# Kernel tuning notes

Measured on AMD Instinct MI355X. Metric: run time of the kernel, lower is better.

Reference implementation:

```python
import jax, jax.numpy as jnp
import numpy as np

B, N, H, F = 256, 256, 256, 64   # batch, nodes, hidden, output
NNB = 4                          # neighbors per node (nns - 1)
HEADS = 3
S = 2 ** NNB - 1                 # nonempty subsets for Mobius Choquet
# MASK[s, i] = True iff neighbor i is in subset s (subsets 1..2^n-1)
MASK = jnp.asarray(np.array([[(s >> i) & 1 for i in range(NNB)] for s in range(1, S + 1)], dtype=bool))


def setup_inputs() -> dict:
    key = jax.random.key(0)
    ks = jax.random.split(key, 12)
    w = 0.02
    centers = jnp.arange(N, dtype=jnp.int64)[:, None]
    neigh = jax.random.randint(ks[11], (N, NNB), 0, N).astype(jnp.int64)
    local_edges = jnp.concatenate([centers, neigh], axis=1)[:, None, :]  # [N, 1, 5]
    return {
        "observation": jax.random.normal(ks[0], (B, N, H), jnp.float32),
        "action": jax.random.normal(ks[1], (B, N, H), jnp.float32),
        "V_W1": jax.random.normal(ks[2], (N, H, H), jnp.float32) * w,
        "V_b1": jnp.zeros((N, H), jnp.float32),
        "V_W2": jax.random.normal(ks[3], (N, H, F), jnp.float32) * w,
        "V_b2": jnp.zeros((N, F), jnp.float32),
        "A_W1": jax.random.normal(ks[4], (N, 2 * H, H), jnp.float32) * w,
        "A_b1": jnp.zeros((N, H), jnp.float32),
        "A_W2": jax.random.normal(ks[5], (N, H, F), jnp.float32) * w,
        "A_b2": jnp.zeros((N, F), jnp.float32),
        "chi_m": jax.random.normal(ks[6], (N, HEADS, S), jnp.float32) * w,
        "local_edges": local_edges,
    }


def _mmlp2(x, W1, b1, W2, b2):
    # per-node (multi) 2-layer MLP: first layer ReLU, second linear (act=False)
    h = jax.nn.relu(jnp.einsum('bni,nio->bno', x, W1) + b1)
    return jnp.einsum('bnh,nho->bno', h, W2) + b2


def reference(observation, action, V_W1, V_b1, V_W2, V_b2,
              A_W1, A_b1, A_W2, A_b2, chi_m, local_edges):
    V = _mmlp2(observation, V_W1, V_b1, V_W2, V_b2)                      # [B,N,F]
    A = _mmlp2(jnp.concatenate([observation, action], axis=-1),
               A_W1, A_b1, A_W2, A_b2)                                   # [B,N,F]
    Q = A + V                                                            # [B,N,F]
    centers = local_edges[:, 0, 0]        # [N]
    neigh = local_edges[:, 0, 1:]         # [N, NNB]
    # .data in torch -> detach the gathered neighbor Q-values
    Qn = jax.lax.stop_gradient(Q[:, neigh, :])                           # [B,N,NNB,F]
    # Mobius Choquet: min over each nonempty subset of neighbors
    masked = jnp.where(MASK[None, None, :, :, None], Qn[:, :, None, :, :], jnp.inf)
    mins = masked.min(axis=3)                                            # [B,N,S,F]
    chi = jnp.einsum('bnsf,nhs->bnf', mins, chi_m) / HEADS               # [B,N,F]
    return (chi + Q[:, centers, :]).mean(axis=-1)                        # [B,N]
```

## Files before the change

### kernel.cpp

```cpp
#include <hip/hip_runtime.h>
#include <cstddef>


#define BN 256
#define HD 256
#define FD 64
#define XS 40
#define SLS 268

typedef _Float16 f16x8 __attribute__((ext_vector_type(8)));
typedef _Float16 f16x4 __attribute__((ext_vector_type(4)));
typedef float f32x4 __attribute__((ext_vector_type(4)));

#define GLOAD16(g, l)                                              \
  __builtin_amdgcn_global_load_lds(                                \
      (__attribute__((address_space(1))) void*)(g),                \
      (__attribute__((address_space(3))) void*)(l), 16, 0, 0)

#define WAIT_BAR(VMCNT_STR)                                        \
  asm volatile("s_waitcnt " VMCNT_STR " lgkmcnt(0)" ::: "memory"); \
  __builtin_amdgcn_s_barrier();                                    \
  asm volatile("" ::: "memory");

__device__ __forceinline__ void x_load(const float* xs0, const float* xs1, int n,
                                       int kt, int tid, float4 xr[4]) {
  int kOff = kt * 32;
  const float* xs = (kOff < 256) ? xs0 : xs1;
  int l = tid & 63, w = tid >> 6;
  const float* base = xs + (size_t)n * HD + (kOff & 255) + (l & 7) * 4;
#pragma unroll
  for (int i = 0; i < 4; ++i) {
    int row = w * 32 + i * 8 + (l >> 3);
    xr[i] = *(const float4*)(base + (size_t)row * (BN * HD));
  }
}
__device__ __forceinline__ void x_write(_Float16* Xl, int tid, const float4 xr[4]) {
  int l = tid & 63, w = tid >> 6;
#pragma unroll
  for (int i = 0; i < 4; ++i) {
    int row = w * 32 + i * 8 + (l >> 3);
    f16x4 v;
    v[0] = (_Float16)xr[i].x; v[1] = (_Float16)xr[i].y;
    v[2] = (_Float16)xr[i].z; v[3] = (_Float16)xr[i].w;
    *(f16x4*)(Xl + row * XS + (l & 7) * 4) = v;
  }
}

__device__ __forceinline__ void w_gload(const float* Wg, float* Wl, int ktile,
                                        int w, int lane) {
#pragma unroll
  for (int s = 0; s < 4; ++s) {
    const float* src = Wg + (size_t)(ktile * 32 + w * 4 + s) * HD + lane * 4;
    float* dst = Wl + (w * 4 + s) * 256;
    GLOAD16(src, dst);
  }
}

__device__ __forceinline__ void g1_compute(const float* Wc, const _Float16* Xc,
                                           int lrow, int lk8, int Nbase, int wm1,
                                           f32x4 acc[8][4]) {
  f16x8 b[4];
#pragma unroll
  for (int nf = 0; nf < 4; ++nf) {
    const float* p = Wc + lk8 * 256 + Nbase + nf * 16 + lrow;
    f16x8 t;
#pragma unroll
    for (int j = 0; j < 8; ++j) t[j] = (_Float16)p[j * 256];
    b[nf] = t;
  }
#pragma unroll
  for (int m = 0; m < 8; ++m) {
    f16x8 a = *(const f16x8*)(Xc + (wm1 * 128 + m * 16 + lrow) * XS + lk8);
#pragma unroll
    for (int nf = 0; nf < 4; ++nf)
      acc[m][nf] = __builtin_amdgcn_mfma_f32_16x16x32_f16(a, b[nf], acc[m][nf], 0, 0, 0);
  }
}

template <int NK>
__device__ __forceinline__ void run_gemm1(const float* xs0, const float* xs1,
                                          const float* Wg, int n, int tid,
                                          int lrow, int lk8, int Nbase, int wm1,
                                          int w, int lane,
                                          float* Wl0, float* Wl1,
                                          _Float16* Xl0, _Float16* Xl1,
                                          f32x4 acc[8][4]) {
  float4 xrA[4], xrB[4];
  w_gload(Wg, Wl0, 0, w, lane);
  x_load(xs0, xs1, n, 0, tid, xrA);
  x_load(xs0, xs1, n, 1, tid, xrB);
  x_write(Xl0, tid, xrA);
  __syncthreads();
#pragma unroll 1
  for (int kt = 0; kt < NK - 2; kt += 2) {
    w_gload(Wg, Wl1, kt + 1, w, lane);
    x_load(xs0, xs1, n, kt + 2, tid, xrA);
    g1_compute(Wl0, Xl0, lrow, lk8, Nbase, wm1, acc);
    x_write(Xl1, tid, xrB);
    WAIT_BAR("vmcnt(4)")
    w_gload(Wg, Wl0, kt + 2, w, lane);
    x_load(xs0, xs1, n, kt + 3, tid, xrB);
    g1_compute(Wl1, Xl1, lrow, lk8, Nbase, wm1, acc);
    x_write(Xl0, tid, xrA);
    WAIT_BAR("vmcnt(4)")
  }
  w_gload(Wg, Wl1, NK - 1, w, lane);
  g1_compute(Wl0, Xl0, lrow, lk8, Nbase, wm1, acc);
  x_write(Xl1, tid, xrB);
  WAIT_BAR("vmcnt(0)")
  g1_compute(Wl1, Xl1, lrow, lk8, Nbase, wm1, acc);
}

__device__ __forceinline__ void gemm2_branch(f32x4 acc[8][4], f32x4 acc2[2][4],
                                             const float* W2g, const float* b1g,
                                             float* W_lds, _Float16* slab,
                                             int lrow, int lq, int lk8,
                                             int Nbase, int wm1, int wn1,
                                             int w, int lane) {
#pragma unroll
  for (int s = 0; s < 8; ++s) {
    int off = w * 2048 + s * 256;
    GLOAD16(W2g + off + lane * 4, W_lds + off);
  }
  float bv[4];
#pragma unroll
  for (int nf = 0; nf < 4; ++nf) bv[nf] = b1g[Nbase + nf * 16 + lrow];
#pragma unroll 1
  for (int s = 0; s < 4; ++s) {
    if (wn1 == s) {
#pragma unroll
      for (int m = 0; m < 8; ++m)
#pragma unroll
        for (int nf = 0; nf < 4; ++nf) {
          f16x4 hv;
#pragma unroll
          for (int r = 0; r < 4; ++r)
            hv[r] = (_Float16)fmaxf(acc[m][nf][r] + bv[nf], 0.f);
          *(f16x4*)(slab + (nf * 16 + lrow) * SLS + wm1 * 128 + m * 16 + lq * 4) = hv;
        }
    }
    __syncthreads();
#pragma unroll
    for (int kf = 0; kf < 2; ++kf) {
      f16x8 a[2], bb[4];
#pragma unroll
      for (int mf = 0; mf < 2; ++mf) {
        f16x8 t;
#pragma unroll
        for (int j = 0; j < 8; ++j)
          t[j] = slab[(kf * 32 + lk8 + j) * SLS + w * 32 + mf * 16 + lrow];
        a[mf] = t;
      }
#pragma unroll
      for (int nf = 0; nf < 4; ++nf) {
        const float* p = W_lds + (s * 64 + kf * 32 + lk8) * 64 + nf * 16 + lrow;
        f16x8 t;
#pragma unroll
        for (int j = 0; j < 8; ++j) t[j] = (_Float16)p[j * 64];
        bb[nf] = t;
      }
#pragma unroll
      for (int mf = 0; mf < 2; ++mf)
#pragma unroll
        for (int nf = 0; nf < 4; ++nf)
          acc2[mf][nf] =
              __builtin_amdgcn_mfma_f32_16x16x32_f16(a[mf], bb[nf], acc2[mf][nf], 0, 0, 0);
    }
    __syncthreads();
  }
}

__global__ __launch_bounds__(512, 2) void phase1_kernel(
    const float* __restrict__ obs, const float* __restrict__ act,
    const float* __restrict__ V_W1, const float* __restrict__ V_b1,
    const float* __restrict__ V_W2, const float* __restrict__ V_b2,
    const float* __restrict__ A_W1, const float* __restrict__ A_b1,
    const float* __restrict__ A_W2, const float* __restrict__ A_b2,
    float* __restrict__ Q) {
  __shared__ float W_lds[16384];
  __shared__ __align__(16) _Float16 Xl[2][256 * XS];
  __shared__ __align__(16) _Float16 slab[64 * SLS];
  float* Wl0 = W_lds;
  float* Wl1 = W_lds + 8192;

  int tid = threadIdx.x;
  int l = tid & 63, w = tid >> 6, lane = l;
  int lrow = l & 15, lq = l >> 4, lk8 = lq * 8;
  int wm1 = w >> 2, wn1 = w & 3;
  int Nbase = wn1 * 64;
  int n = blockIdx.x;

  f32x4 acc[8][4];
  f32x4 acc2[2][4];
#pragma unroll
  for (int i = 0; i < 2; ++i)
#pragma unroll
    for (int j = 0; j < 4; ++j) acc2[i][j] = (f32x4){0.f, 0.f, 0.f, 0.f};

#pragma unroll
  for (int m = 0; m < 8; ++m)
#pragma unroll
    for (int nf = 0; nf < 4; ++nf) acc[m][nf] = (f32x4){0.f, 0.f, 0.f, 0.f};
  run_gemm1<8>(obs, obs, V_W1 + (size_t)n * HD * HD, n, tid, lrow, lk8, Nbase,
               wm1, w, lane, Wl0, Wl1, Xl[0], Xl[1], acc);
  __syncthreads();
  gemm2_branch(acc, acc2, V_W2 + (size_t)n * HD * FD, V_b1 + n * HD,
               W_lds, slab, lrow, lq, lk8, Nbase, wm1, wn1, w, lane);

#pragma unroll
  for (int m = 0; m < 8; ++m)
#pragma unroll
    for (int nf = 0; nf < 4; ++nf) acc[m][nf] = (f32x4){0.f, 0.f, 0.f, 0.f};
  run_gemm1<16>(obs, act, A_W1 + (size_t)n * 2 * HD * HD, n, tid, lrow, lk8, Nbase,
                wm1, w, lane, Wl0, Wl1, Xl[0], Xl[1], acc);
  __syncthreads();
  gemm2_branch(acc, acc2, A_W2 + (size_t)n * HD * FD, A_b1 + n * HD,
               W_lds, slab, lrow, lq, lk8, Nbase, wm1, wn1, w, lane);

  const float* vb2 = V_b2 + n * FD;
  const float* ab2 = A_b2 + n * FD;
#pragma unroll
  for (int mf = 0; mf < 2; ++mf)
#pragma unroll
    for (int nf = 0; nf < 4; ++nf) {
      int f = nf * 16 + lrow;
      float bias = vb2[f] + ab2[f];
#pragma unroll
      for (int rr = 0; rr < 4; ++rr) {
        int row = w * 32 + mf * 16 + lq * 4 + rr;
        Q[(size_t)row * (BN * FD) + n * FD + f] = acc2[mf][nf][rr] + bias;
      }
    }
}

__global__ __launch_bounds__(256) void phase2_kernel(const float* __restrict__ Q,
                                                     const float* __restrict__ chi_m,
                                                     const int* __restrict__ le,
                                                     float* __restrict__ out) {
  int b = blockIdx.x;
  int n = threadIdx.x;
  int step = (le[5] == 1) ? 1 : 2;
  const int* e = le + n * 5 * step;
  int c  = e[0 * step] & (BN - 1);
  int n0 = e[1 * step] & (BN - 1);
  int n1 = e[2 * step] & (BN - 1);
  int n2 = e[3 * step] & (BN - 1);
  int n3 = e[4 * step] & (BN - 1);
  const float* ch = chi_m + n * 45;
  float cm[15];
#pragma unroll
  for (int s = 0; s < 15; ++s) cm[s] = (ch[s] + ch[15 + s] + ch[30 + s]) * (1.f / 3.f);
  const float* qb = Q + (size_t)b * (BN * FD);
  const float* q0 = qb + n0 * FD;
  const float* q1 = qb + n1 * FD;
  const float* q2 = qb + n2 * FD;
  const float* q3 = qb + n3 * FD;
  const float* qc = qb + c * FD;
  float acc = 0.f;
#pragma unroll
  for (int f = 0; f < FD; f += 4) {
    float4 v0 = *(const float4*)(q0 + f);
    float4 v1 = *(const float4*)(q1 + f);
    float4 v2 = *(const float4*)(q2 + f);
    float4 v3 = *(const float4*)(q3 + f);
    float4 vc = *(const float4*)(qc + f);
    const float* p0 = (const float*)&v0;
    const float* p1 = (const float*)&v1;
    const float* p2 = (const float*)&v2;
    const float* p3 = (const float*)&v3;
    const float* pc = (const float*)&vc;
#pragma unroll
    for (int u = 0; u < 4; ++u) {
      float a = p0[u], bq = p1[u], cq = p2[u], d = p3[u];
      float m01 = fminf(a, bq), m02 = fminf(a, cq), m03 = fminf(a, d);
      float m12 = fminf(bq, cq), m13 = fminf(bq, d), m23 = fminf(cq, d);
      float m012 = fminf(m01, cq), m013 = fminf(m01, d);
      float m023 = fminf(m02, d),  m123 = fminf(m12, d);
      float m0123 = fminf(m01, m23);
      float chi = cm[0] * a   + cm[1] * bq   + cm[2] * m01  + cm[3] * cq
                + cm[4] * m02 + cm[5] * m12  + cm[6] * m012 + cm[7] * d
                + cm[8] * m03 + cm[9] * m13  + cm[10] * m013 + cm[11] * m23
                + cm[12] * m023 + cm[13] * m123 + cm[14] * m0123;
      acc += chi + pc[u];
    }
  }
  out[b * BN + n] = acc * (1.f / 64.f);
}

extern "C" void kernel_launch(void* const* d_in, const int* in_sizes, int n_in,
                              void* d_out, int out_size, void* d_ws, size_t ws_size,
                              hipStream_t stream) {
  (void)in_sizes; (void)n_in; (void)out_size; (void)ws_size;
  const float* obs  = (const float*)d_in[0];
  const float* act  = (const float*)d_in[1];
  const float* V_W1 = (const float*)d_in[2];
  const float* V_b1 = (const float*)d_in[3];
  const float* V_W2 = (const float*)d_in[4];
  const float* V_b2 = (const float*)d_in[5];
  const float* A_W1 = (const float*)d_in[6];
  const float* A_b1 = (const float*)d_in[7];
  const float* A_W2 = (const float*)d_in[8];
  const float* A_b2 = (const float*)d_in[9];
  const float* chim = (const float*)d_in[10];
  const int*   le   = (const int*)d_in[11];
  float* Q   = (float*)d_ws;
  float* out = (float*)d_out;

  phase1_kernel<<<dim3(256), dim3(512), 0, stream>>>(obs, act, V_W1, V_b1, V_W2, V_b2,
                                                     A_W1, A_b1, A_W2, A_b2, Q);
  phase2_kernel<<<dim3(256), dim3(256), 0, stream>>>(Q, chim, le, out);
}
```

Baseline: 117.5 us.

## Use triple-buffered weight ring, prefetch W2 during GEMM1 tail, swizzle LDS

Measured after the change: 116.5 us. Within noise of the previous version (-0.9%).

```diff
diff --git a/kernel.cpp b/kernel.cpp
--- a/kernel.cpp
+++ b/kernel.cpp
@@ -46,26 +46,41 @@
   }
 }
 
-__device__ __forceinline__ void w_gload(const float* Wg, float* Wl, int ktile,
-                                        int w, int lane) {
+__device__ __forceinline__ void w1_gload(const float* __restrict__ Wg, float* Wl,
+                                         int ktile, int w, int lane) {
 #pragma unroll
   for (int s = 0; s < 4; ++s) {
-    const float* src = Wg + (size_t)(ktile * 32 + w * 4 + s) * HD + lane * 4;
-    float* dst = Wl + (w * 4 + s) * 256;
-    GLOAD16(src, dst);
+    int rl = w * 4 + s;
+    int swz = ((rl >> 3) & 3) << 4;
+    const float* src = Wg + (size_t)(ktile * 32 + rl) * HD + ((lane * 4) ^ swz);
+    GLOAD16(src, Wl + rl * HD);
+  }
+}
+
+__device__ __forceinline__ void w2_gload_half(const float* __restrict__ W2g, float* chunk,
+                                              int half, int w, int lane) {
+#pragma unroll
+  for (int s = 0; s < 4; ++s) {
+    int rl = (w * 4 + s) * 4;
+    int swz = ((rl >> 3) & 3) << 4;
+    const float* src = W2g + (size_t)(half * 128 + rl + (lane >> 4)) * FD
+                       + (((lane & 15) * 4) ^ swz);
+    GLOAD16(src, chunk + rl * FD);
   }
 }
 
 __device__ __forceinline__ void g1_compute(const float* Wc, const _Float16* Xc,
-                                           int lrow, int lk8, int Nbase, int wm1,
+                                           int lrow, int lq, int Nbase, int wm1,
                                            f32x4 acc[8][4]) {
+  int lk8 = lq * 8;
+  const float* wbase = Wc + lk8 * 256;
   f16x8 b[4];
 #pragma unroll
   for (int nf = 0; nf < 4; ++nf) {
-    const float* p = Wc + lk8 * 256 + Nbase + nf * 16 + lrow;
+    int col = (Nbase + nf * 16 + lrow) ^ (lq << 4);
     f16x8 t;
 #pragma unroll
-    for (int j = 0; j < 8; ++j) t[j] = (_Float16)p[j * 256];
+    for (int j = 0; j < 8; ++j) t[j] = (_Float16)wbase[j * 256 + col];
     b[nf] = t;
   }
 #pragma unroll
@@ -79,49 +94,56 @@
 
 template <int NK>
 __device__ __forceinline__ void run_gemm1(const float* xs0, const float* xs1,
-                                          const float* Wg, int n, int tid,
-                                          int lrow, int lk8, int Nbase, int wm1,
-                                          int w, int lane,
-                                          float* Wl0, float* Wl1,
-                                          _Float16* Xl0, _Float16* Xl1,
+                                          const float* __restrict__ Wg,
+                                          const float* __restrict__ W2g,
+                                          int n, int tid, int lrow, int lq,
+                                          int Nbase, int wm1, int w, int lane,
+                                          float* Wring, _Float16* Xl0, _Float16* Xl1,
                                           f32x4 acc[8][4]) {
+  float* w0 = Wring;
+  float* w1 = Wring + 8192;
+  float* w2 = Wring + 16384;
   float4 xrA[4], xrB[4];
-  w_gload(Wg, Wl0, 0, w, lane);
   x_load(xs0, xs1, n, 0, tid, xrA);
+  w1_gload(Wg, w0, 0, w, lane);
   x_load(xs0, xs1, n, 1, tid, xrB);
+  w1_gload(Wg, w1, 1, w, lane);
   x_write(Xl0, tid, xrA);
-  __syncthreads();
+  WAIT_BAR("vmcnt(8)")
 #pragma unroll 1
-  for (int kt = 0; kt < NK - 2; kt += 2) {
-    w_gload(Wg, Wl1, kt + 1, w, lane);
-    x_load(xs0, xs1, n, kt + 2, tid, xrA);
-    g1_compute(Wl0, Xl0, lrow, lk8, Nbase, wm1, acc);
-    x_write(Xl1, tid, xrB);
-    WAIT_BAR("vmcnt(4)")
-    w_gload(Wg, Wl0, kt + 2, w, lane);
-    x_load(xs0, xs1, n, kt + 3, tid, xrB);
-    g1_compute(Wl1, Xl1, lrow, lk8, Nbase, wm1, acc);
-    x_write(Xl0, tid, xrA);
-    WAIT_BAR("vmcnt(4)")
-  }
-  w_gload(Wg, Wl1, NK - 1, w, lane);
-  g1_compute(Wl0, Xl0, lrow, lk8, Nbase, wm1, acc);
-  x_write(Xl1, tid, xrB);
-  WAIT_BAR("vmcnt(0)")
-  g1_compute(Wl1, Xl1, lrow, lk8, Nbase, wm1, acc);
+  for (int kt = 0; kt < NK; kt += 2) {
+    if (kt + 2 < NK) {
+      x_load(xs0, xs1, n, kt + 2, tid, xrA);
+      w1_gload(Wg, w2, kt + 2, w, lane);
+    } else {
+      w2_gload_half(W2g, w2, 0, w, lane);
+    }
+    g1_compute(w0, Xl0, lrow, lq, Nbase, wm1, acc);
+    if (kt + 1 < NK) x_write(Xl1, tid, xrB);
+    if (kt < NK - 2) { WAIT_BAR("vmcnt(8)") }
+    else             { WAIT_BAR("vmcnt(4)") }
+    { float* t = w0; w0 = w1; w1 = w2; w2 = t; }
+    if (kt + 3 < NK) {
+      x_load(xs0, xs1, n, kt + 3, tid, xrB);
+      w1_gload(Wg, w2, kt + 3, w, lane);
+    } else {
+      w2_gload_half(W2g, w2, 1, w, lane);
+    }
+    g1_compute(w0, Xl1, lrow, lq, Nbase, wm1, acc);
+    if (kt + 2 < NK) {
+      x_write(Xl0, tid, xrA);
+      WAIT_BAR("vmcnt(8)")
+    }
+    { float* t = w0; w0 = w1; w1 = w2; w2 = t; }
+  }
 }
 
 __device__ __forceinline__ void gemm2_branch(f32x4 acc[8][4], f32x4 acc2[2][4],
-                                             const float* W2g, const float* b1g,
-                                             float* W_lds, _Float16* slab,
-                                             int lrow, int lq, int lk8,
-                                             int Nbase, int wm1, int wn1,
-                                             int w, int lane) {
-#pragma unroll
-  for (int s = 0; s < 8; ++s) {
-    int off = w * 2048 + s * 256;
-    GLOAD16(W2g + off + lane * 4, W_lds + off);
-  }
+                                             const float* cA, const float* cB,
+                                             const float* __restrict__ b1g,
+                                             _Float16* slab, int lrow, int lq,
+                                             int Nbase, int wm1, int wn1, int w) {
+  int lk8 = lq * 8;
   float bv[4];
 #pragma unroll
   for (int nf = 0; nf < 4; ++nf) bv[nf] = b1g[Nbase + nf * 16 + lrow];
@@ -142,21 +164,23 @@
     __syncthreads();
 #pragma unroll
     for (int kf = 0; kf < 2; ++kf) {
-      f16x8 a[2], bb[4];
+      const int r0 = s * 64 + kf * 32;
+      const float* wb2 = ((r0 < 128) ? cA : cB) + ((r0 & 127) + lk8) * FD;
+      f16x8 a2[2], bb[4];
 #pragma unroll
       for (int mf = 0; mf < 2; ++mf) {
         f16x8 t;
 #pragma unroll
         for (int j = 0; j < 8; ++j)
           t[j] = slab[(kf * 32 + lk8 + j) * SLS + w * 32 + mf * 16 + lrow];
-        a[mf] = t;
+        a2[mf] = t;
       }
 #pragma unroll
       for (int nf = 0; nf < 4; ++nf) {
-        const float* p = W_lds + (s * 64 + kf * 32 + lk8) * 64 + nf * 16 + lrow;
+        int col = (nf * 16 + lrow) ^ (lq << 4);
         f16x8 t;
 #pragma unroll
-        for (int j = 0; j < 8; ++j) t[j] = (_Float16)p[j * 64];
+        for (int j = 0; j < 8; ++j) t[j] = (_Float16)wb2[j * FD + col];
         bb[nf] = t;
       }
 #pragma unroll
@@ -164,7 +188,7 @@
 #pragma unroll
         for (int nf = 0; nf < 4; ++nf)
           acc2[mf][nf] =
-              __builtin_amdgcn_mfma_f32_16x16x32_f16(a[mf], bb[nf], acc2[mf][nf], 0, 0, 0);
+              __builtin_amdgcn_mfma_f32_16x16x32_f16(a2[mf], bb[nf], acc2[mf][nf], 0, 0, 0);
     }
     __syncthreads();
   }
@@ -177,15 +201,15 @@
     const float* __restrict__ A_W1, const float* __restrict__ A_b1,
     const float* __restrict__ A_W2, const float* __restrict__ A_b2,
     float* __restrict__ Q) {
-  __shared__ float W_lds[16384];
-  __shared__ __align__(16) _Float16 Xl[2][256 * XS];
-  __shared__ __align__(16) _Float16 slab[64 * SLS];
-  float* Wl0 = W_lds;
-  float* Wl1 = W_lds + 8192;
+  __shared__ __align__(16) float smem[34816];
+  float* Wring = smem;
+  _Float16* Xl0 = (_Float16*)(smem + 24576);
+  _Float16* Xl1 = Xl0 + 10240;
+  _Float16* slab = (_Float16*)(smem + 24576);
 
   int tid = threadIdx.x;
   int l = tid & 63, w = tid >> 6, lane = l;
-  int lrow = l & 15, lq = l >> 4, lk8 = lq * 8;
+  int lrow = l & 15, lq = l >> 4;
   int wm1 = w >> 2, wn1 = w & 3;
   int Nbase = wn1 * 64;
   int n = blockIdx.x;
@@ -201,21 +225,21 @@
   for (int m = 0; m < 8; ++m)
 #pragma unroll
     for (int nf = 0; nf < 4; ++nf) acc[m][nf] = (f32x4){0.f, 0.f, 0.f, 0.f};
-  run_gemm1<8>(obs, obs, V_W1 + (size_t)n * HD * HD, n, tid, lrow, lk8, Nbase,
-               wm1, w, lane, Wl0, Wl1, Xl[0], Xl[1], acc);
+  run_gemm1<8>(obs, obs, V_W1 + (size_t)n * HD * HD, V_W2 + (size_t)n * HD * FD,
+               n, tid, lrow, lq, Nbase, wm1, w, lane, Wring, Xl0, Xl1, acc);
   __syncthreads();
-  gemm2_branch(acc, acc2, V_W2 + (size_t)n * HD * FD, V_b1 + n * HD,
-               W_lds, slab, lrow, lq, lk8, Nbase, wm1, wn1, w, lane);
+  gemm2_branch(acc, acc2, Wring + 16384 , Wring ,
+               V_b1 + n * HD, slab, lrow, lq, Nbase, wm1, wn1, w);
 
 #pragma unroll
   for (int m = 0; m < 8; ++m)
 #pragma unroll
     for (int nf = 0; nf < 4; ++nf) acc[m][nf] = (f32x4){0.f, 0.f, 0.f, 0.f};
-  run_gemm1<16>(obs, act, A_W1 + (size_t)n * 2 * HD * HD, n, tid, lrow, lk8, Nbase,
-                wm1, w, lane, Wl0, Wl1, Xl[0], Xl[1], acc);
+  run_gemm1<16>(obs, act, A_W1 + (size_t)n * 2 * HD * HD, A_W2 + (size_t)n * HD * FD,
+                n, tid, lrow, lq, Nbase, wm1, w, lane, Wring, Xl0, Xl1, acc);
   __syncthreads();
-  gemm2_branch(acc, acc2, A_W2 + (size_t)n * HD * FD, A_b1 + n * HD,
-               W_lds, slab, lrow, lq, lk8, Nbase, wm1, wn1, w, lane);
+  gemm2_branch(acc, acc2, Wring + 8192 , Wring + 16384 ,
+               A_b1 + n * HD, slab, lrow, lq, Nbase, wm1, wn1, w);
 
   const float* vb2 = V_b2 + n * FD;
   const float* ab2 = A_b2 + n * FD;
```
